# Kernel optimization log

Measured on AMD Instinct MI355X. Metric: run time of the kernel, lower is better.

The kernel has to match this reference:

```python
import jax, jax.numpy as jnp
import numpy as np

N_HEADS = 16
HEAD_DIM = 64
ROPE_BASE = 10000.0
EPS = 1e-6


def _rope_tables(T, hd, dtype):
    inv_freq = 1.0 / (ROPE_BASE ** (jnp.arange(0, hd, 2, dtype=jnp.float32) / hd))
    freqs = jnp.arange(T, dtype=jnp.float32)[:, None] * inv_freq[None, :]  # [T, hd/2]
    cos = jnp.cos(freqs)[None, :, None, :].astype(dtype)  # [1,T,1,hd/2]
    sin = jnp.sin(freqs)[None, :, None, :].astype(dtype)
    return cos, sin


def _apply_rope(x, cos, sin):
    d = x.shape[-1] // 2
    x1, x2 = x[..., :d], x[..., d:]
    return jnp.concatenate([x1 * cos + x2 * sin, -x1 * sin + x2 * cos], axis=-1)


def setup_inputs() -> dict:
    key = jax.random.key(0)
    k1, k2, k3, k4 = jax.random.split(key, 4)
    B, T, C = 4, 1024, 1024
    x = jax.random.normal(k1, (B, T, C), dtype=jnp.float32)
    W_qkv = jax.random.normal(k2, (3 * C, C), dtype=jnp.float32) * (1.0 / np.sqrt(C))
    W_out = jax.random.normal(k3, (C, C), dtype=jnp.float32) * (1.0 / np.sqrt(C))
    # learnable per-head curvature, init = exp(randn) * base_curvature (base=1.0)
    hyp_k = jnp.exp(jax.random.normal(k4, (1, N_HEADS, 1, 1), dtype=jnp.float32))
    return {"x": x, "W_qkv": W_qkv, "W_out": W_out, "hyp_k": hyp_k}


def reference(x, W_qkv, W_out, hyp_k):
    B, T, C = x.shape
    H, hd = N_HEADS, HEAD_DIM
    qkv = x @ W_qkv.T  # [B,T,3C]
    q, k, v = jnp.split(qkv, 3, axis=-1)
    q = q.reshape(B, T, H, hd)
    k = k.reshape(B, T, H, hd)
    v = v.reshape(B, T, H, hd)

    cos, sin = _rope_tables(T, hd, x.dtype)
    q = _apply_rope(q, cos, sin)
    k = _apply_rope(k, cos, sin)

    # [B,H,T,hd]
    q = q.transpose(0, 2, 1, 3)
    k = k.transpose(0, 2, 1, 3)
    v = v.transpose(0, 2, 1, 3)

    # Lorentz lift: x0 = sqrt(k + ||x||^2); inner = -x0*y0 + <x,y>;
    # dist = sqrt(k) * arccosh(-inner / k)  (geoopt Lorentz convention)
    kc = hyp_k[:, :, :, 0]  # [1,H,1]
    q0 = jnp.sqrt(kc + jnp.sum(q * q, axis=-1))  # [B,H,T]
    k0 = jnp.sqrt(kc + jnp.sum(k * k, axis=-1))  # [B,H,T]
    inner = jnp.einsum('bhld,bhsd->bhls', q, k) - q0[..., None] * k0[:, :, None, :]
    arg = jnp.maximum(-inner / hyp_k, 1.0 + EPS)
    dis = jnp.sqrt(hyp_k) * jnp.arccosh(arg)  # [B,H,L,S]

    attn_weight = 1.0 / (EPS + dis)
    causal = jnp.tril(jnp.ones((T, T), dtype=bool))
    attn_weight = jnp.where(causal, attn_weight, -jnp.inf)
    attn = jax.nn.softmax(attn_weight, axis=-1)
    out = jnp.einsum('bhls,bhsd->bhld', attn, v)  # [B,H,T,hd]
    out = out.transpose(0, 2, 1, 3).reshape(B, T, C)
    return out @ W_out.T
```

## Files before the change

kernel.cpp:

```cpp
#include <hip/hip_runtime.h>

#define B_ 4
#define T_ 1024
#define C_ 1024
#define H_ 16
#define HD_ 64

typedef short bf16x8 __attribute__((ext_vector_type(8)));
typedef float f32x4 __attribute__((ext_vector_type(4)));

__device__ __forceinline__ ushort f2bf(float f) {
    union { float f; unsigned u; } v; v.f = f;
    unsigned u = v.u;
    unsigned r = (u + 0x7fffu + ((u >> 16) & 1u)) >> 16;
    return (ushort)r;
}

__device__ __forceinline__ f32x4 mfma16(bf16x8 a, bf16x8 b, f32x4 c) {
    return __builtin_amdgcn_mfma_f32_16x16x32_bf16(a, b, c, 0, 0, 0);
}

__device__ __forceinline__ bf16x8 lds_frag(const ushort* base, int row, int byteoff) {
    int addr = (row * 128 + byteoff) ^ ((row & 7) << 4);
    uint4 u = *(const uint4*)((const char*)base + addr);
    return __builtin_bit_cast(bf16x8, u);
}

__device__ __forceinline__ bf16x8 lds_frag_v(const ushort* base, int d, int byteoff) {
    int addr = (d * 128 + byteoff) ^ ((((d & 7) ^ (d >> 3)) & 7) << 4);
    uint4 u = *(const uint4*)((const char*)base + addr);
    return __builtin_bit_cast(bf16x8, u);
}

__device__ __forceinline__ bf16x8 lds_frag_p(const ushort* base, int row, int byteoff) {
    int addr = (row * 128 + byteoff) ^ (((row >> 2) & 3) << 5);
    uint4 u = *(const uint4*)((const char*)base + addr);
    return __builtin_bit_cast(bf16x8, u);
}

__device__ __forceinline__ void stage_tile(ushort* sdst, const ushort* gsrc, int ld, int tid) {
#pragma unroll
    for (int it = 0; it < 2; ++it) {
        int c = tid + it * 256;
        int row = c >> 3, off = c & 7;
        uint4 v = *(const uint4*)(gsrc + (size_t)row * ld + off * 8);
        int addr = (c * 16) ^ ((row & 7) << 4);
        *(uint4*)((char*)sdst + addr) = v;
    }
}

__global__ void cast_bf16(const float* __restrict__ in, ushort* __restrict__ out, int n) {
    int i = (blockIdx.x * 256 + threadIdx.x) * 4;
    if (i >= n) return;
    float4 v = *(const float4*)(in + i);
    ushort4 o = make_ushort4(f2bf(v.x), f2bf(v.y), f2bf(v.z), f2bf(v.w));
    *(ushort4*)(out + i) = o;
}

__global__ __launch_bounds__(256) void gemm_qkv(
    const ushort* __restrict__ Xb, const ushort* __restrict__ Wb,
    const float* __restrict__ hyp,
    ushort* __restrict__ Qo, ushort* __restrict__ Ko, ushort* __restrict__ Vo,
    float* __restrict__ q0g, float* __restrict__ k0g)
{
    __shared__ ushort As[64 * 64];
    __shared__ ushort Bs[64 * 64];
    const int tid = threadIdx.x, lane = tid & 63, wv = tid >> 6;
    const int m0 = blockIdx.x * 64, n0 = blockIdx.y * 64;

    f32x4 acc[4] = {};
    for (int kt = 0; kt < C_ / 64; ++kt) {
        stage_tile(As, Xb + (size_t)m0 * C_ + kt * 64, C_, tid);
        stage_tile(Bs, Wb + (size_t)n0 * C_ + kt * 64, C_, tid);
        __syncthreads();
#pragma unroll
        for (int ks = 0; ks < 2; ++ks) {
            bf16x8 a = lds_frag(As, wv * 16 + (lane & 15), ks * 64 + ((lane >> 4) << 4));
#pragma unroll
            for (int cf = 0; cf < 4; ++cf) {
                bf16x8 b = lds_frag(Bs, cf * 16 + (lane & 15), ks * 64 + ((lane >> 4) << 4));
                acc[cf] = mfma16(a, b, acc[cf]);
            }
        }
        __syncthreads();
    }

    const int sector = n0 >> 10;
    const int h = (n0 & 1023) >> 6;
    const float kc = hyp[h];
    const float inv_k = 1.0f / kc;

    float out[4][4];
#pragma unroll
    for (int cf = 0; cf < 4; ++cf)
#pragma unroll
        for (int r = 0; r < 4; ++r) out[cf][r] = acc[cf][r];

    if (sector < 2) {
#pragma unroll
        for (int cf = 0; cf < 2; ++cf) {
            const float j = (float)(cf * 16 + (lane & 15));
            const float invf = __expf(-0.28782313662425572f * j);
#pragma unroll
            for (int r = 0; r < 4; ++r) {
                int m = m0 + wv * 16 + ((lane >> 4) << 2) + r;
                int t = m & (T_ - 1);
                float ang = (float)t * invf;
                float sn, cs; __sincosf(ang, &sn, &cs);
                float x1 = out[cf][r], x2 = out[cf + 2][r];
                out[cf][r]     =  x1 * cs + x2 * sn;
                out[cf + 2][r] = -x1 * sn + x2 * cs;
            }
        }
    }

#pragma unroll
    for (int r = 0; r < 4; ++r) {
        int m = m0 + wv * 16 + ((lane >> 4) << 2) + r;
        int b = m >> 10, t = m & (T_ - 1);
        int bh = b * H_ + h;
        size_t base = ((size_t)bh * T_ + t) * HD_;
        float nrm = 0.f;
#pragma unroll
        for (int cf = 0; cf < 4; ++cf) {
            int d = cf * 16 + (lane & 15);
            float v = out[cf][r];
            nrm += v * v;
            ushort bv = f2bf(sector == 1 ? v * inv_k : v);
            if (sector == 0)      Qo[base + d] = bv;
            else if (sector == 1) Ko[base + d] = bv;
            else                  Vo[base + d] = bv;
        }
        if (sector < 2) {
#pragma unroll
            for (int mk = 1; mk < 16; mk <<= 1) nrm += __shfl_xor(nrm, mk);
            if ((lane & 15) == 0) {
                float v0 = sqrtf(kc + nrm);
                if (sector == 0) q0g[(size_t)bh * T_ + t] = v0;
                else             k0g[(size_t)bh * T_ + t] = v0 * inv_k;
            }
        }
    }
}

__global__ __launch_bounds__(256, 2) void attn_fwd(
    const ushort* __restrict__ Q, const ushort* __restrict__ K, const ushort* __restrict__ V,
    const float* __restrict__ q0g, const float* __restrict__ k0g,
    const float* __restrict__ hyp, ushort* __restrict__ AO)
{
    __shared__ ushort Ks[64 * 64];
    __shared__ ushort Vts[64 * 64];
    __shared__ ushort Ps[8][16 * 64];
    __shared__ float k0s[64];

    const int tid = threadIdx.x, lane = tid & 63, wv = tid >> 6;
    const int pr = blockIdx.x >> 6;
    const int bh = blockIdx.x & 63;
    const int h = bh & (H_ - 1);
    const int qa = pr, qb = 15 - pr, nt = qb + 1;
    const float c3 = sqrtf(hyp[h]) * 0.48045301391820142f;
    const float e3 = 6.931471805599453e-07f;

    const ushort* Kb = K + (size_t)bh * T_ * HD_;
    const ushort* Vb = V + (size_t)bh * T_ * HD_;

    bf16x8 aqA[2], aqB[2];
    {
        const ushort* qA = Q + ((size_t)bh * T_ + qa * 64 + wv * 16 + (lane & 15)) * HD_;
        const ushort* qB = Q + ((size_t)bh * T_ + qb * 64 + wv * 16 + (lane & 15)) * HD_;
#pragma unroll
        for (int ks = 0; ks < 2; ++ks) {
            aqA[ks] = __builtin_bit_cast(bf16x8, *(const uint4*)(qA + ks * 32 + ((lane >> 4) << 3)));
            aqB[ks] = __builtin_bit_cast(bf16x8, *(const uint4*)(qB + ks * 32 + ((lane >> 4) << 3)));
        }
    }
    float q0A[4], q0B[4];
#pragma unroll
    for (int r = 0; r < 4; ++r) {
        int rr = wv * 16 + ((lane >> 4) << 2) + r;
        q0A[r] = q0g[(size_t)bh * T_ + qa * 64 + rr];
        q0B[r] = q0g[(size_t)bh * T_ + qb * 64 + rr];
    }

    f32x4 oaccA[4] = {}, oaccB[4] = {};
    float lpA[4] = {}, lpB[4] = {};

    const int krow = tid >> 3, koff = tid & 7;
    const int sp = tid >> 3, dc = tid & 7;
    uint4 kv0, kv1, vv0, vv1;
    float kz = 0.f;
    auto issue = [&](int s0) {
        kv0 = *(const uint4*)(Kb + (size_t)(s0 + krow) * HD_ + koff * 8);
        kv1 = *(const uint4*)(Kb + (size_t)(s0 + 32 + krow) * HD_ + koff * 8);
        vv0 = *(const uint4*)(Vb + (size_t)(s0 + 2 * sp) * HD_ + dc * 8);
        vv1 = *(const uint4*)(Vb + (size_t)(s0 + 2 * sp + 1) * HD_ + dc * 8);
        if (tid < 64) kz = k0g[(size_t)bh * T_ + s0 + tid];
    };

    auto geom = [&](const f32x4* sc, const float* q0, const float* k0r, float p[4][4]) {
#pragma unroll
        for (int r = 0; r < 4; ++r)
#pragma unroll
            for (int sf = 0; sf < 4; ++sf) {
                float arg = fmaf(q0[r], k0r[sf], -sc[sf][r]);
                arg = fmaxf(arg, 1.0f + 1e-6f);
                float t = fmaf(arg, arg, -1.0f);
                float u = arg + __builtin_amdgcn_sqrtf(t);
                float l2 = __builtin_amdgcn_logf(u);
                float w2 = fmaf(l2, c3, e3);
                float rv = fminf(__builtin_amdgcn_rcpf(w2), 30.0f);
                p[sf][r] = __builtin_amdgcn_exp2f(rv);
            }
    };
    auto mask_diag = [&](float p[4][4]) {
        const int qloc = wv * 16 + ((lane >> 4) << 2);
#pragma unroll
        for (int r = 0; r < 4; ++r)
#pragma unroll
            for (int sf = 0; sf < 4; ++sf)
                if (sf * 16 + (lane & 15) > qloc + r) p[sf][r] = 0.f;
    };
    auto pv_step = [&](float p[4][4], ushort* ps, const bf16x8 (&vf)[2][4],
                       f32x4* oacc, float* lp) {
#pragma unroll
        for (int r = 0; r < 4; ++r) {
            int row = ((lane >> 4) << 2) + r;
#pragma unroll
            for (int sf = 0; sf < 4; ++sf) {
                int addr = (row * 128 + (sf * 16 + (lane & 15)) * 2) ^ (((row >> 2) & 3) << 5);
                *(ushort*)((char*)ps + addr) = f2bf(p[sf][r]);
            }
            lp[r] += (p[0][r] + p[1][r]) + (p[2][r] + p[3][r]);
        }
#pragma unroll
        for (int ks = 0; ks < 2; ++ks) {
            bf16x8 ap = lds_frag_p(ps, lane & 15, ks * 64 + ((lane >> 4) << 4));
#pragma unroll
            for (int df = 0; df < 4; ++df)
                oacc[df] = mfma16(ap, vf[ks][df], oacc[df]);
        }
    };

    issue(0);

    for (int it = 0; it < nt; ++it) {
        const bool actA = (it <= qa);
        __syncthreads();
        {
            *(uint4*)((char*)Ks + ((tid * 16) ^ ((krow & 7) << 4))) = kv0;
            int c1 = tid + 256;
            *(uint4*)((char*)Ks + ((c1 * 16) ^ (((c1 >> 3) & 7) << 4))) = kv1;
            union { uint4 v; ushort u[8]; } a, b;
            a.v = vv0; b.v = vv1;
#pragma unroll
            for (int j = 0; j < 8; ++j) {
                int d = dc * 8 + j;
                uint pack = (uint)a.u[j] | ((uint)b.u[j] << 16);
                *(uint*)((char*)Vts + ((d * 128 + sp * 4) ^ (((j ^ dc) & 7) << 4))) = pack;
            }
            if (tid < 64) k0s[tid] = kz;
        }
        if (it + 1 < nt) issue((it + 1) * 64);
        __syncthreads();

        bf16x8 bk[2][4];
#pragma unroll
        for (int ks = 0; ks < 2; ++ks)
#pragma unroll
            for (int sf = 0; sf < 4; ++sf)
                bk[ks][sf] = lds_frag(Ks, sf * 16 + (lane & 15), ks * 64 + ((lane >> 4) << 4));

        float k0r[4];
#pragma unroll
        for (int sf = 0; sf < 4; ++sf) k0r[sf] = k0s[sf * 16 + (lane & 15)];

        f32x4 scB[4] = {};
#pragma unroll
        for (int ks = 0; ks < 2; ++ks)
#pragma unroll
            for (int sf = 0; sf < 4; ++sf)
                scB[sf] = mfma16(aqB[ks], bk[ks][sf], scB[sf]);
        f32x4 scA[4] = {};
        if (actA) {
#pragma unroll
            for (int ks = 0; ks < 2; ++ks)
#pragma unroll
                for (int sf = 0; sf < 4; ++sf)
                    scA[sf] = mfma16(aqA[ks], bk[ks][sf], scA[sf]);
        }

        bf16x8 vf[2][4];
#pragma unroll
        for (int ks = 0; ks < 2; ++ks)
#pragma unroll
            for (int df = 0; df < 4; ++df)
                vf[ks][df] = lds_frag_v(Vts, df * 16 + (lane & 15), ks * 64 + ((lane >> 4) << 4));

        float pB[4][4];
        geom(scB, q0B, k0r, pB);
        if (it == qb) mask_diag(pB);
        pv_step(pB, Ps[wv * 2 + 1], vf, oaccB, lpB);

        if (actA) {
            float pA[4][4];
            geom(scA, q0A, k0r, pA);
            if (it == qa) mask_diag(pA);
            pv_step(pA, Ps[wv * 2 + 0], vf, oaccA, lpA);
        }
    }

    const int b = bh >> 4;
    auto epi = [&](f32x4* oacc, float* lp, int qt) {
#pragma unroll
        for (int r = 0; r < 4; ++r) {
            float s = lp[r];
#pragma unroll
            for (int mk = 1; mk < 16; mk <<= 1) s += __shfl_xor(s, mk);
            float invl = __builtin_amdgcn_rcpf(s);
            int t = qt * 64 + wv * 16 + ((lane >> 4) << 2) + r;
            size_t base = ((size_t)b * T_ + t) * C_ + h * HD_;
#pragma unroll
            for (int df = 0; df < 4; ++df)
                AO[base + df * 16 + (lane & 15)] = f2bf(oacc[df][r] * invl);
        }
    };
    epi(oaccA, lpA, qa);
    epi(oaccB, lpB, qb);
}

__global__ __launch_bounds__(256) void gemm_out(
    const ushort* __restrict__ Ab, const ushort* __restrict__ Wb, float* __restrict__ Out)
{
    __shared__ ushort As[64 * 64];
    __shared__ ushort Bs[64 * 64];
    const int tid = threadIdx.x, lane = tid & 63, wv = tid >> 6;
    const int m0 = blockIdx.x * 64, n0 = blockIdx.y * 64;

    f32x4 acc[4] = {};
    for (int kt = 0; kt < C_ / 64; ++kt) {
        stage_tile(As, Ab + (size_t)m0 * C_ + kt * 64, C_, tid);
        stage_tile(Bs, Wb + (size_t)n0 * C_ + kt * 64, C_, tid);
        __syncthreads();
#pragma unroll
        for (int ks = 0; ks < 2; ++ks) {
            bf16x8 a = lds_frag(As, wv * 16 + (lane & 15), ks * 64 + ((lane >> 4) << 4));
#pragma unroll
            for (int cf = 0; cf < 4; ++cf) {
                bf16x8 b = lds_frag(Bs, cf * 16 + (lane & 15), ks * 64 + ((lane >> 4) << 4));
                acc[cf] = mfma16(a, b, acc[cf]);
            }
        }
        __syncthreads();
    }
#pragma unroll
    for (int cf = 0; cf < 4; ++cf)
#pragma unroll
        for (int r = 0; r < 4; ++r) {
            int m = m0 + wv * 16 + ((lane >> 4) << 2) + r;
            int n = n0 + cf * 16 + (lane & 15);
            Out[(size_t)m * C_ + n] = acc[cf][r];
        }
}

extern "C" void kernel_launch(void* const* d_in, const int* in_sizes, int n_in,
                              void* d_out, int out_size, void* d_ws, size_t ws_size,
                              hipStream_t stream)
{
    const float* x    = (const float*)d_in[0];
    const float* wqkv = (const float*)d_in[1];
    const float* wout = (const float*)d_in[2];
    const float* hyp  = (const float*)d_in[3];

    char* ws = (char*)d_ws;
    ushort* xb    = (ushort*)(ws + 0);
    ushort* wqkvb = (ushort*)(ws + 8388608);
    ushort* woutb = (ushort*)(ws + 14680064);
    ushort* Qb    = (ushort*)(ws + 16777216);
    ushort* Kb    = (ushort*)(ws + 25165824);
    ushort* Vb    = (ushort*)(ws + 33554432);
    ushort* Ab    = (ushort*)(ws + 41943040);
    float*  q0    = (float*)(ws + 50331648);
    float*  k0    = (float*)(ws + 50593792);

    cast_bf16<<<4096, 256, 0, stream>>>(x, xb, 4194304);
    cast_bf16<<<3072, 256, 0, stream>>>(wqkv, wqkvb, 3145728);
    cast_bf16<<<1024, 256, 0, stream>>>(wout, woutb, 1048576);

    gemm_qkv<<<dim3(64, 48), 256, 0, stream>>>(xb, wqkvb, hyp, Qb, Kb, Vb, q0, k0);
    attn_fwd<<<512, 256, 0, stream>>>(Qb, Kb, Vb, q0, k0, hyp, Ab);
    gemm_out<<<dim3(64, 16), 256, 0, stream>>>(Ab, woutb, (float*)d_out);
}
```

Measured before the change: 109.0 us.

## Enlarge GEMM tiles to 128x128 with direct global-to-LDS loads

Both projection GEMMs now use 128x128 output tiles, with each wave computing a 64x64 sub-tile through a 4x4 grid of MFMA fragments. Operands are staged with global_load_lds using an XOR swizzle that matches the existing fragment reads. The aim is to raise arithmetic intensity and cut LDS and global traffic per FLOP, and to skip the register round-trip during staging. The trade-off is fewer blocks, which lowers occupancy on the output GEMM, plus higher register pressure from the 16 accumulators.

```diff
diff --git a/kernel.cpp b/kernel.cpp
--- a/kernel.cpp
+++ b/kernel.cpp
@@ -36,6 +36,19 @@
     int addr = (row * 128 + byteoff) ^ (((row >> 2) & 3) << 5);
     uint4 u = *(const uint4*)((const char*)base + addr);
     return __builtin_bit_cast(bf16x8, u);
+}
+
+__device__ __forceinline__ void stage128(ushort* sbase, const ushort* gtile, int wv, int lane) {
+    const int srow = lane >> 3;
+    const ushort* g0 = gtile + (size_t)srow * C_ + ((((lane & 7) ^ srow)) << 3);
+#pragma unroll
+    for (int i = 0; i < 4; ++i) {
+        int w = wv * 4 + i;
+        const ushort* g = g0 + (size_t)(w * 8) * C_;
+        ushort* l = sbase + w * 512;
+        __builtin_amdgcn_global_load_lds((const __attribute__((address_space(1))) void*)g,
+                                         (__attribute__((address_space(3))) void*)l, 16, 0, 0);
+    }
 }
 
 __device__ __forceinline__ void stage_tile(ushort* sdst, const ushort* gsrc, int ld, int tid) {
@@ -63,81 +76,91 @@
     ushort* __restrict__ Qo, ushort* __restrict__ Ko, ushort* __restrict__ Vo,
     float* __restrict__ q0g, float* __restrict__ k0g)
 {
-    __shared__ ushort As[64 * 64];
-    __shared__ ushort Bs[64 * 64];
+    __shared__ ushort As[128 * 64];
+    __shared__ ushort Bs[128 * 64];
     const int tid = threadIdx.x, lane = tid & 63, wv = tid >> 6;
-    const int m0 = blockIdx.x * 64, n0 = blockIdx.y * 64;
-
-    f32x4 acc[4] = {};
+    const int wr = wv >> 1, wc = wv & 1;
+    const int m0 = blockIdx.x * 128, n0 = blockIdx.y * 128;
+
+    f32x4 acc[4][4] = {};
     for (int kt = 0; kt < C_ / 64; ++kt) {
-        stage_tile(As, Xb + (size_t)m0 * C_ + kt * 64, C_, tid);
-        stage_tile(Bs, Wb + (size_t)n0 * C_ + kt * 64, C_, tid);
+        stage128(As, Xb + (size_t)m0 * C_ + kt * 64, wv, lane);
+        stage128(Bs, Wb + (size_t)n0 * C_ + kt * 64, wv, lane);
         __syncthreads();
 #pragma unroll
         for (int ks = 0; ks < 2; ++ks) {
-            bf16x8 a = lds_frag(As, wv * 16 + (lane & 15), ks * 64 + ((lane >> 4) << 4));
-#pragma unroll
-            for (int cf = 0; cf < 4; ++cf) {
-                bf16x8 b = lds_frag(Bs, cf * 16 + (lane & 15), ks * 64 + ((lane >> 4) << 4));
-                acc[cf] = mfma16(a, b, acc[cf]);
-            }
+            bf16x8 af[4], bfr[4];
+#pragma unroll
+            for (int mf = 0; mf < 4; ++mf)
+                af[mf] = lds_frag(As, wr * 64 + mf * 16 + (lane & 15), ks * 64 + ((lane >> 4) << 4));
+#pragma unroll
+            for (int nf = 0; nf < 4; ++nf)
+                bfr[nf] = lds_frag(Bs, wc * 64 + nf * 16 + (lane & 15), ks * 64 + ((lane >> 4) << 4));
+#pragma unroll
+            for (int mf = 0; mf < 4; ++mf)
+#pragma unroll
+                for (int nf = 0; nf < 4; ++nf)
+                    acc[mf][nf] = mfma16(af[mf], bfr[nf], acc[mf][nf]);
         }
         __syncthreads();
     }
 
     const int sector = n0 >> 10;
-    const int h = (n0 & 1023) >> 6;
+    const int h = ((n0 & 1023) >> 6) + wc;
     const float kc = hyp[h];
     const float inv_k = 1.0f / kc;
-
-    float out[4][4];
-#pragma unroll
-    for (int cf = 0; cf < 4; ++cf)
-#pragma unroll
-        for (int r = 0; r < 4; ++r) out[cf][r] = acc[cf][r];
-
-    if (sector < 2) {
-#pragma unroll
-        for (int cf = 0; cf < 2; ++cf) {
-            const float j = (float)(cf * 16 + (lane & 15));
-            const float invf = __expf(-0.28782313662425572f * j);
-#pragma unroll
-            for (int r = 0; r < 4; ++r) {
-                int m = m0 + wv * 16 + ((lane >> 4) << 2) + r;
-                int t = m & (T_ - 1);
-                float ang = (float)t * invf;
-                float sn, cs; __sincosf(ang, &sn, &cs);
-                float x1 = out[cf][r], x2 = out[cf + 2][r];
-                out[cf][r]     =  x1 * cs + x2 * sn;
-                out[cf + 2][r] = -x1 * sn + x2 * cs;
-            }
-        }
-    }
-
-#pragma unroll
-    for (int r = 0; r < 4; ++r) {
-        int m = m0 + wv * 16 + ((lane >> 4) << 2) + r;
-        int b = m >> 10, t = m & (T_ - 1);
-        int bh = b * H_ + h;
-        size_t base = ((size_t)bh * T_ + t) * HD_;
-        float nrm = 0.f;
-#pragma unroll
-        for (int cf = 0; cf < 4; ++cf) {
-            int d = cf * 16 + (lane & 15);
-            float v = out[cf][r];
-            nrm += v * v;
-            ushort bv = f2bf(sector == 1 ? v * inv_k : v);
-            if (sector == 0)      Qo[base + d] = bv;
-            else if (sector == 1) Ko[base + d] = bv;
-            else                  Vo[base + d] = bv;
-        }
+    float invf[2];
+    invf[0] = __expf(-0.28782313662425572f * (float)(lane & 15));
+    invf[1] = __expf(-0.28782313662425572f * (float)(16 + (lane & 15)));
+
+#pragma unroll
+    for (int mf = 0; mf < 4; ++mf) {
+        float o[4][4];
+#pragma unroll
+        for (int nf = 0; nf < 4; ++nf)
+#pragma unroll
+            for (int r = 0; r < 4; ++r) o[nf][r] = acc[mf][nf][r];
+
         if (sector < 2) {
 #pragma unroll
-            for (int mk = 1; mk < 16; mk <<= 1) nrm += __shfl_xor(nrm, mk);
-            if ((lane & 15) == 0) {
-                float v0 = sqrtf(kc + nrm);
-                if (sector == 0) q0g[(size_t)bh * T_ + t] = v0;
-                else             k0g[(size_t)bh * T_ + t] = v0 * inv_k;
+            for (int p = 0; p < 2; ++p) {
+#pragma unroll
+                for (int r = 0; r < 4; ++r) {
+                    int m = m0 + wr * 64 + mf * 16 + ((lane >> 4) << 2) + r;
+                    int t = m & (T_ - 1);
+                    float sn, cs; __sincosf((float)t * invf[p], &sn, &cs);
+                    float x1 = o[p][r], x2 = o[p + 2][r];
+                    o[p][r]     =  x1 * cs + x2 * sn;
+                    o[p + 2][r] = -x1 * sn + x2 * cs;
+                }
+            }
+        }
+
+#pragma unroll
+        for (int r = 0; r < 4; ++r) {
+            int m = m0 + wr * 64 + mf * 16 + ((lane >> 4) << 2) + r;
+            int b = m >> 10, t = m & (T_ - 1);
+            int bh = b * H_ + h;
+            size_t base = ((size_t)bh * T_ + t) * HD_;
+            float nrm = 0.f;
+#pragma unroll
+            for (int nf = 0; nf < 4; ++nf) {
+                int d = nf * 16 + (lane & 15);
+                float v = o[nf][r];
+                nrm += v * v;
+                ushort bv = f2bf(sector == 1 ? v * inv_k : v);
+                if (sector == 0)      Qo[base + d] = bv;
+                else if (sector == 1) Ko[base + d] = bv;
+                else                  Vo[base + d] = bv;
+            }
+            if (sector < 2) {
+#pragma unroll
+                for (int mk = 1; mk < 16; mk <<= 1) nrm += __shfl_xor(nrm, mk);
+                if ((lane & 15) == 0) {
+                    float v0 = sqrtf(kc + nrm);
+                    if (sector == 0) q0g[(size_t)bh * T_ + t] = v0;
+                    else             k0g[(size_t)bh * T_ + t] = v0 * inv_k;
+                }
             }
         }
     }
@@ -331,34 +354,44 @@
 __global__ __launch_bounds__(256) void gemm_out(
     const ushort* __restrict__ Ab, const ushort* __restrict__ Wb, float* __restrict__ Out)
 {
-    __shared__ ushort As[64 * 64];
-    __shared__ ushort Bs[64 * 64];
+    __shared__ ushort As[128 * 64];
+    __shared__ ushort Bs[128 * 64];
     const int tid = threadIdx.x, lane = tid & 63, wv = tid >> 6;
-    const int m0 = blockIdx.x * 64, n0 = blockIdx.y * 64;
-
-    f32x4 acc[4] = {};
+    const int wr = wv >> 1, wc = wv & 1;
+    const int m0 = blockIdx.x * 128, n0 = blockIdx.y * 128;
+
+    f32x4 acc[4][4] = {};
     for (int kt = 0; kt < C_ / 64; ++kt) {
-        stage_tile(As, Ab + (size_t)m0 * C_ + kt * 64, C_, tid);
-        stage_tile(Bs, Wb + (size_t)n0 * C_ + kt * 64, C_, tid);
+        stage128(As, Ab + (size_t)m0 * C_ + kt * 64, wv, lane);
+        stage128(Bs, Wb + (size_t)n0 * C_ + kt * 64, wv, lane);
         __syncthreads();
 #pragma unroll
         for (int ks = 0; ks < 2; ++ks) {
-            bf16x8 a = lds_frag(As, wv * 16 + (lane & 15), ks * 64 + ((lane >> 4) << 4));
-#pragma unroll
-            for (int cf = 0; cf < 4; ++cf) {
-                bf16x8 b = lds_frag(Bs, cf * 16 + (lane & 15), ks * 64 + ((lane >> 4) << 4));
-                acc[cf] = mfma16(a, b, acc[cf]);
-            }
-        }
-        __syncthreads();
-    }
-#pragma unroll
-    for (int cf = 0; cf < 4; ++cf)
+            bf16x8 af[4], bfr[4];
+#pragma unroll
+            for (int mf = 0; mf < 4; ++mf)
+                af[mf] = lds_frag(As, wr * 64 + mf * 16 + (lane & 15), ks * 64 + ((lane >> 4) << 4));
+#pragma unroll
+            for (int nf = 0; nf < 4; ++nf)
+                bfr[nf] = lds_frag(Bs, wc * 64 + nf * 16 + (lane & 15), ks * 64 + ((lane >> 4) << 4));
+#pragma unroll
+            for (int mf = 0; mf < 4; ++mf)
+#pragma unroll
+                for (int nf = 0; nf < 4; ++nf)
+                    acc[mf][nf] = mfma16(af[mf], bfr[nf], acc[mf][nf]);
+        }
+        __syncthreads();
+    }
+#pragma unroll
+    for (int mf = 0; mf < 4; ++mf)
 #pragma unroll
         for (int r = 0; r < 4; ++r) {
-            int m = m0 + wv * 16 + ((lane >> 4) << 2) + r;
-            int n = n0 + cf * 16 + (lane & 15);
-            Out[(size_t)m * C_ + n] = acc[cf][r];
+            int m = m0 + wr * 64 + mf * 16 + ((lane >> 4) << 2) + r;
+#pragma unroll
+            for (int nf = 0; nf < 4; ++nf) {
+                int n = n0 + wc * 64 + nf * 16 + (lane & 15);
+                Out[(size_t)m * C_ + n] = acc[mf][nf][r];
+            }
         }
 }
 
@@ -386,7 +419,7 @@
     cast_bf16<<<3072, 256, 0, stream>>>(wqkv, wqkvb, 3145728);
     cast_bf16<<<1024, 256, 0, stream>>>(wout, woutb, 1048576);
 
-    gemm_qkv<<<dim3(64, 48), 256, 0, stream>>>(xb, wqkvb, hyp, Qb, Kb, Vb, q0, k0);
+    gemm_qkv<<<dim3(32, 24), 256, 0, stream>>>(xb, wqkvb, hyp, Qb, Kb, Vb, q0, k0);
     attn_fwd<<<512, 256, 0, stream>>>(Qb, Kb, Vb, q0, k0, hyp, Ab);
-    gemm_out<<<dim3(64, 16), 256, 0, stream>>>(Ab, woutb, (float*)d_out);
-}
+    gemm_out<<<dim3(32, 8), 256, 0, stream>>>(Ab, woutb, (float*)d_out);
+}
```

New measurement: 117.6 us. 7.9% more time.
